# Kernel optimization log

Measured on AMD Instinct MI355X. Metric: run time of the kernel, lower is better.

## Reference

```python
import jax, jax.numpy as jnp
import numpy as np

D_MODEL = 1024
NUM_HEAD = 16
D_HEAD = D_MODEL // NUM_HEAD
D_FFN = 4096
EPS = 1e-6


def setup_inputs() -> dict:
    key = jax.random.key(0)
    ks = jax.random.split(key, 8)
    s = 0.02
    return {
        "x": jax.random.normal(ks[0], (2, 2048, D_MODEL), dtype=jnp.float32),
        "wq": jax.random.normal(ks[1], (D_MODEL, D_MODEL), dtype=jnp.float32) * s,
        "bq": jnp.zeros((D_MODEL,), jnp.float32),
        "ln1_a": jax.random.uniform(ks[2], (D_MODEL,), dtype=jnp.float32),
        "ln1_b": jnp.zeros((D_MODEL,), jnp.float32),
        "ln2_a": jax.random.uniform(ks[3], (D_MODEL,), dtype=jnp.float32),
        "ln2_b": jnp.zeros((D_MODEL,), jnp.float32),
        "w1": jax.random.normal(ks[4], (D_FFN, D_MODEL), dtype=jnp.float32) * s,
        "b1": jnp.zeros((D_FFN,), jnp.float32),
        "w2": jax.random.normal(ks[5], (D_MODEL, D_FFN), dtype=jnp.float32) * s,
        "b2": jnp.zeros((D_MODEL,), jnp.float32),
    }


def _laynorm(x, a, b):
    # torch.std is unbiased (ddof=1); original divides by (std + eps)
    mean = jnp.mean(x, axis=-1, keepdims=True)
    std = jnp.std(x, axis=-1, keepdims=True, ddof=1)
    return a * ((x - mean) / (std + EPS)) + b


def reference(x, wq, bq, ln1_a, ln1_b, ln2_a, ln2_b, w1, b1, w2, b2):
    B, S, D = x.shape
    # NOTE: original applies Wq to Q, K, and V (Wk/Wv unused); Wo never applied.
    h = x @ wq.T + bq                      # [B,S,D]
    h = h.reshape(B, S, NUM_HEAD, D_HEAD)  # q = k = v = h
    scale = 1.0 / jnp.sqrt(jnp.float32(D_HEAD))
    scores = jnp.einsum("bqhd,bkhd->bhqk", h, h) * scale  # [B,H,S,S]
    att = jax.nn.softmax(scores, axis=-1)
    att_out = jnp.einsum("bhqk,bkhd->bqhd", att, h).reshape(B, S, D)
    # dropout is identity at inference
    x1 = _laynorm(x + att_out, ln1_a, ln1_b)
    ffn = jax.nn.relu(x1 @ w1.T + b1) @ w2.T + b2
    return _laynorm(x1 + ffn, ln2_a, ln2_b)
```

## Files before the change

kernel.cpp:

```cpp
#include <hip/hip_runtime.h>

typedef __bf16 bf16v8 __attribute__((ext_vector_type(8)));
typedef float f32x4 __attribute__((ext_vector_type(4)));

#define AS1 __attribute__((address_space(1)))
#define AS3 __attribute__((address_space(3)))

__device__ __forceinline__ void gl_lds16(const void* g, void* s) {
  __builtin_amdgcn_global_load_lds((const AS1 void*)g, (AS3 void*)s, 16, 0, 0);
}

__device__ __forceinline__ unsigned short f2b(float f) {
  union { float f; unsigned u; } v; v.f = f;
  unsigned r = v.u + 0x7fffu + ((v.u >> 16) & 1u);
  return (unsigned short)(r >> 16);
}

__device__ __forceinline__ float bitsf(unsigned u) {
  union { unsigned u; float f; } v; v.u = u;
  return v.f;
}

__global__ __launch_bounds__(256) void cvt_all(const float* __restrict__ x,
                                               const float* __restrict__ wq,
                                               const float* __restrict__ w1,
                                               const float* __restrict__ w2,
                                               unsigned short* __restrict__ xb,
                                               unsigned short* __restrict__ wqb,
                                               unsigned short* __restrict__ w1b,
                                               unsigned short* __restrict__ w2b) {
  int bid = blockIdx.x;
  const float* in;
  unsigned short* out;
  int base;
  if (bid < 4096)       { in = x;  out = xb;  base = bid; }
  else if (bid < 5120)  { in = wq; out = wqb; base = bid - 4096; }
  else if (bid < 9216)  { in = w1; out = w1b; base = bid - 5120; }
  else                  { in = w2; out = w2b; base = bid - 9216; }
  long i = ((long)base * 256 + threadIdx.x) * 4;
  float4 v = *(const float4*)(in + i);
  ushort4 u = make_ushort4(f2b(v.x), f2b(v.y), f2b(v.z), f2b(v.w));
  *(ushort4*)(out + i) = u;
}

template <int RELU, int SPLIT>
__global__ __launch_bounds__(512, 2) void gemm256p(const unsigned short* __restrict__ A,
                                                   const unsigned short* __restrict__ B,
                                                   const float* __restrict__ bias,
                                                   unsigned short* __restrict__ Cb,
                                                   int M, int N, int K, int Ks) {
  __shared__ unsigned short As[2][2][8192];
  __shared__ unsigned short Bs[2][2][8192];

  const int tid = threadIdx.x;
  const int wave = tid >> 6, lane = tid & 63;
  const int wr = wave >> 2, wc = wave & 3;
  const int g = lane >> 4, l15 = lane & 15;

  const int gx = gridDim.x;
  const int nwg = gx * gridDim.y;
  const int lin = blockIdx.y * gx + blockIdx.x;
  const int cpx = nwg >> 3;
  const int swz = (lin & 7) * cpx + (lin >> 3);
  const long m0 = (long)(swz / gx) * 256;
  const long n0 = (long)(swz % gx) * 256;
  const int kBase = blockIdx.z * Ks;

  const int srow = lane >> 2;
  const int schunk = ((lane & 3) ^ ((lane >> 3) & 3)) * 8;

  auto stA = [&](int buf, int kk, int kb) {
#pragma unroll
    for (int j = 0; j < 2; ++j) {
      const int seg = wave * 2 + j;
      gl_lds16(A + (m0 + seg * 16 + srow) * (long)K + kb + kk * 32 + schunk,
               &As[buf][kk][seg * 512]);
    }
  };
  auto stB = [&](int buf, int kk, int kb) {
#pragma unroll
    for (int j = 0; j < 2; ++j) {
      const int seg = wave * 2 + j;
      gl_lds16(B + (n0 + seg * 16 + srow) * (long)K + kb + kk * 32 + schunk,
               &Bs[buf][kk][seg * 512]);
    }
  };

  const int sel = (l15 >> 1) & 3;
  const int colA = (g ^ sel) << 3;

  f32x4 acc[8][4] = {};
  const int nt = Ks >> 6;

  stA(0, 0, kBase); stB(0, 0, kBase); stA(0, 1, kBase); stB(0, 1, kBase);
  asm volatile("s_waitcnt vmcnt(4)" ::: "memory");
  __builtin_amdgcn_s_barrier();

  int cur = 0;
  for (int t = 0; t < nt; ++t) {
    const bool pf = (t + 1 < nt);
    const int kbn = kBase + ((t + 1) << 6);
    bf16v8 af[8], b0, b1, b2, b3;

#pragma unroll
    for (int m = 0; m < 8; ++m)
      af[m] = *(const bf16v8*)&As[cur][0][(wr * 128 + m * 16 + l15) * 32 + colA];
    b0 = *(const bf16v8*)&Bs[cur][0][(wc * 64 + 0 * 16 + l15) * 32 + colA];
    b1 = *(const bf16v8*)&Bs[cur][0][(wc * 64 + 1 * 16 + l15) * 32 + colA];
    if (pf) stA(cur ^ 1, 0, kbn);
    __builtin_amdgcn_s_barrier();
    asm volatile("s_waitcnt lgkmcnt(0)" ::: "memory");
    __builtin_amdgcn_s_setprio(1);
#pragma unroll
    for (int m = 0; m < 8; ++m) {
      acc[m][0] = __builtin_amdgcn_mfma_f32_16x16x32_bf16(af[m], b0, acc[m][0], 0, 0, 0);
      acc[m][1] = __builtin_amdgcn_mfma_f32_16x16x32_bf16(af[m], b1, acc[m][1], 0, 0, 0);
    }
    __builtin_amdgcn_s_setprio(0);
    __builtin_amdgcn_s_barrier();

    b2 = *(const bf16v8*)&Bs[cur][0][(wc * 64 + 2 * 16 + l15) * 32 + colA];
    b3 = *(const bf16v8*)&Bs[cur][0][(wc * 64 + 3 * 16 + l15) * 32 + colA];
    if (pf) stB(cur ^ 1, 0, kbn);
    __builtin_amdgcn_s_barrier();
    asm volatile("s_waitcnt lgkmcnt(0)" ::: "memory");
    __builtin_amdgcn_s_setprio(1);
#pragma unroll
    for (int m = 0; m < 8; ++m) {
      acc[m][2] = __builtin_amdgcn_mfma_f32_16x16x32_bf16(af[m], b2, acc[m][2], 0, 0, 0);
      acc[m][3] = __builtin_amdgcn_mfma_f32_16x16x32_bf16(af[m], b3, acc[m][3], 0, 0, 0);
    }
    __builtin_amdgcn_s_setprio(0);
    if (pf) { asm volatile("s_waitcnt vmcnt(4)" ::: "memory"); }
    else    { asm volatile("s_waitcnt vmcnt(0)" ::: "memory"); }
    __builtin_amdgcn_s_barrier();

#pragma unroll
    for (int m = 0; m < 8; ++m)
      af[m] = *(const bf16v8*)&As[cur][1][(wr * 128 + m * 16 + l15) * 32 + colA];
    b0 = *(const bf16v8*)&Bs[cur][1][(wc * 64 + 0 * 16 + l15) * 32 + colA];
    b1 = *(const bf16v8*)&Bs[cur][1][(wc * 64 + 1 * 16 + l15) * 32 + colA];
    if (pf) stA(cur ^ 1, 1, kbn);
    __builtin_amdgcn_s_barrier();
    asm volatile("s_waitcnt lgkmcnt(0)" ::: "memory");
    __builtin_amdgcn_s_setprio(1);
#pragma unroll
    for (int m = 0; m < 8; ++m) {
      acc[m][0] = __builtin_amdgcn_mfma_f32_16x16x32_bf16(af[m], b0, acc[m][0], 0, 0, 0);
      acc[m][1] = __builtin_amdgcn_mfma_f32_16x16x32_bf16(af[m], b1, acc[m][1], 0, 0, 0);
    }
    __builtin_amdgcn_s_setprio(0);
    __builtin_amdgcn_s_barrier();

    b2 = *(const bf16v8*)&Bs[cur][1][(wc * 64 + 2 * 16 + l15) * 32 + colA];
    b3 = *(const bf16v8*)&Bs[cur][1][(wc * 64 + 3 * 16 + l15) * 32 + colA];
    if (pf) stB(cur ^ 1, 1, kbn);
    __builtin_amdgcn_s_barrier();
    asm volatile("s_waitcnt lgkmcnt(0)" ::: "memory");
    __builtin_amdgcn_s_setprio(1);
#pragma unroll
    for (int m = 0; m < 8; ++m) {
      acc[m][2] = __builtin_amdgcn_mfma_f32_16x16x32_bf16(af[m], b2, acc[m][2], 0, 0, 0);
      acc[m][3] = __builtin_amdgcn_mfma_f32_16x16x32_bf16(af[m], b3, acc[m][3], 0, 0, 0);
    }
    __builtin_amdgcn_s_setprio(0);
    if (pf) { asm volatile("s_waitcnt vmcnt(4)" ::: "memory"); }
    else    { asm volatile("s_waitcnt vmcnt(0)" ::: "memory"); }
    __builtin_amdgcn_s_barrier();

    cur ^= 1;
  }

  const long zoff = SPLIT ? (long)blockIdx.z * M * (long)N : 0;
#pragma unroll
  for (int m = 0; m < 8; ++m)
#pragma unroll
    for (int n = 0; n < 4; ++n) {
      long col = n0 + wc * 64 + n * 16 + l15;
      float bv = SPLIT ? 0.f : bias[col];
      long rowb = m0 + wr * 128 + m * 16 + g * 4;
#pragma unroll
      for (int i = 0; i < 4; ++i) {
        float v = acc[m][n][i] + bv;
        if (RELU) v = fmaxf(v, 0.f);
        Cb[zoff + (rowb + i) * (long)N + col] = f2b(v);
      }
    }
}

__global__ __launch_bounds__(256) void merge4_bias(const unsigned short* __restrict__ p,
                                                   const float* __restrict__ bias,
                                                   unsigned short* __restrict__ out) {
  const long PS = 4096L * 1024L;
  long i = ((long)blockIdx.x * 256 + threadIdx.x) * 8;
  int col = (int)(i & 1023);
  float4 b0 = *(const float4*)(bias + col);
  float4 b1 = *(const float4*)(bias + col + 4);
  float acc[8] = {b0.x, b0.y, b0.z, b0.w, b1.x, b1.y, b1.z, b1.w};
#pragma unroll
  for (int sp = 0; sp < 4; ++sp) {
    uint4 u = *(const uint4*)(p + sp * PS + i);
    unsigned r[4] = {u.x, u.y, u.z, u.w};
#pragma unroll
    for (int j = 0; j < 4; ++j) {
      acc[j * 2]     += bitsf(r[j] << 16);
      acc[j * 2 + 1] += bitsf(r[j] & 0xffff0000u);
    }
  }
  unsigned short res[8];
#pragma unroll
  for (int j = 0; j < 8; ++j) res[j] = f2b(acc[j]);
  *(uint4*)(out + i) = *(uint4*)res;
}

__global__ __launch_bounds__(512, 2) void attn_kernel(const unsigned short* __restrict__ h,
                                                      unsigned short* __restrict__ o) {
  const int id = blockIdx.y * 8 + blockIdx.x;
  const int bh = id & 31;
  const int b = bh >> 4, head = bh & 15;
  const int q0 = (id >> 5) * 256;
  const unsigned short* hb = h + (long)b * 2048 * 1024 + head * 64;

  __shared__ unsigned short smem[2 * 19712];

  const int tid = threadIdx.x, wave = tid >> 6, lane = tid & 63;
  const int grp = wave >> 2, wg = wave & 3;
  const int g = lane >> 4, l15 = lane & 15;
  const int vcb = wg * 16;
  unsigned short* Ks0 = smem + grp * 19712;
  unsigned short* VTb = Ks0 + 8192;

  for (int idx = wg * 64 + lane; idx < 16 * 72; idx += 256) {
    unsigned short v = (idx < 72) ? (unsigned short)0x3F80 : (unsigned short)0;
    VTb[64 * 72 + idx] = v;
    VTb[5760 + 64 * 72 + idx] = v;
  }

  const float C1 = 0.18033688011112042f;

  bf16v8 qf[4][2];
#pragma unroll
  for (int qt = 0; qt < 4; ++qt)
#pragma unroll
    for (int d = 0; d < 2; ++d) {
      bf16v8 q = *(const bf16v8*)(hb + (long)(q0 + wg * 64 + qt * 16 + l15) * 1024 + d * 32 + g * 8);
#pragma unroll
      for (int j = 0; j < 8; ++j) q[j] = (__bf16)((float)q[j] * C1);
      qf[qt][d] = q;
    }

  const int krow = lane >> 3;
  const int kcol = ((lane & 7) ^ (krow & 7)) << 3;

  const int kl = lane;
  const int vpos = ((kl >> 5) << 5) + (((kl & 15) >> 2) << 3) + (((kl >> 4) & 1) << 2) + (kl & 3);

#pragma unroll
  for (int s = 0; s < 2; ++s) {
    int seg = wg * 2 + s;
    gl_lds16(hb + (long)(grp * 64 + seg * 8 + krow) * 1024 + kcol, Ks0 + seg * 512);
  }
  uint4 va0, va1;
  {
    const unsigned short* vg = hb + (long)(grp * 64 + lane) * 1024 + vcb;
    va0 = *(const uint4*)vg;
    va1 = *(const uint4*)(vg + 8);
  }
  {
    unsigned short vv[16];
    *(uint4*)&vv[0] = va0;
    *(uint4*)&vv[8] = va1;
#pragma unroll
    for (int j = 0; j < 16; ++j) VTb[(vcb + j) * 72 + vpos] = vv[j];
  }
  __syncthreads();

  f32x4 accO[4][4] = {};
  f32x4 accL[4] = {};

  int cur = 0;
  for (int t = 0; t < 16; ++t) {
    if (t < 15) {
      const int k0n = ((t + 1) * 2 + grp) * 64;
#pragma unroll
      for (int s = 0; s < 2; ++s) {
        int seg = wg * 2 + s;
        gl_lds16(hb + (long)(k0n + seg * 8 + krow) * 1024 + kcol, Ks0 + (cur ^ 1) * 4096 + seg * 512);
      }
      const unsigned short* vg = hb + (long)(k0n + lane) * 1024 + vcb;
      va0 = *(const uint4*)vg;
      va1 = *(const uint4*)(vg + 8);
    }

    const unsigned short* Kc = Ks0 + cur * 4096;
    f32x4 sf[4][4] = {};
#pragma unroll
    for (int d = 0; d < 2; ++d) {
#pragma unroll
      for (int kt = 0; kt < 4; ++kt) {
        int r = kt * 16 + l15;
        bf16v8 kf = *(const bf16v8*)&Kc[r * 64 + ((((d << 2) + g) ^ (r & 7)) << 3)];
#pragma unroll
        for (int qt = 0; qt < 4; ++qt)
          sf[kt][qt] = __builtin_amdgcn_mfma_f32_16x16x32_bf16(kf, qf[qt][d], sf[kt][qt], 0, 0, 0);
      }
    }

    bf16v8 pa[4][2];
#pragma unroll
    for (int qt = 0; qt < 4; ++qt) {
      float pe[4][4];
#pragma unroll
      for (int kt = 0; kt < 4; ++kt)
#pragma unroll
        for (int i = 0; i < 4; ++i)
          pe[kt][i] = __builtin_amdgcn_exp2f(sf[kt][qt][i]);
#pragma unroll
      for (int i = 0; i < 4; ++i) {
        pa[qt][0][i]     = (__bf16)pe[0][i];
        pa[qt][0][i + 4] = (__bf16)pe[1][i];
        pa[qt][1][i]     = (__bf16)pe[2][i];
        pa[qt][1][i + 4] = (__bf16)pe[3][i];
      }
    }

    const unsigned short* VTc = VTb + cur * 5760;
#pragma unroll
    for (int ks = 0; ks < 2; ++ks) {
      bf16v8 vl = *(const bf16v8*)&VTc[(64 + l15) * 72 + ks * 32 + g * 8];
#pragma unroll
      for (int dt = 0; dt < 4; ++dt) {
        bf16v8 vf = *(const bf16v8*)&VTc[(dt * 16 + l15) * 72 + ks * 32 + g * 8];
#pragma unroll
        for (int qt = 0; qt < 4; ++qt)
          accO[qt][dt] = __builtin_amdgcn_mfma_f32_16x16x32_bf16(pa[qt][ks], vf, accO[qt][dt], 0, 0, 0);
      }
#pragma unroll
      for (int qt = 0; qt < 4; ++qt)
        accL[qt] = __builtin_amdgcn_mfma_f32_16x16x32_bf16(pa[qt][ks], vl, accL[qt], 0, 0, 0);
    }

    if (t < 15) {
      unsigned short vv[16];
      *(uint4*)&vv[0] = va0;
      *(uint4*)&vv[8] = va1;
      unsigned short* VTn = VTb + (cur ^ 1) * 5760;
#pragma unroll
      for (int j = 0; j < 16; ++j) VTn[(vcb + j) * 72 + vpos] = vv[j];
    }
    __syncthreads();
    cur ^= 1;
  }

  float* redO = (float*)smem;
  float* redL = (float*)smem + 16384;
  if (grp == 1) {
#pragma unroll
    for (int qt = 0; qt < 4; ++qt)
#pragma unroll
      for (int i = 0; i < 4; ++i) {
        int r = wg * 64 + qt * 16 + g * 4 + i;
#pragma unroll
        for (int dt = 0; dt < 4; ++dt)
          redO[r * 64 + dt * 16 + l15] = accO[qt][dt][i];
        if (l15 == 0) redL[r] = accL[qt][i];
      }
  }
  __syncthreads();
  if (grp == 0) {
#pragma unroll
    for (int qt = 0; qt < 4; ++qt)
#pragma unroll
      for (int i = 0; i < 4; ++i) {
        int r = wg * 64 + qt * 16 + g * 4 + i;
#pragma unroll
        for (int dt = 0; dt < 4; ++dt)
          accO[qt][dt][i] += redO[r * 64 + dt * 16 + l15];
        accL[qt][i] += redL[r];
      }
#pragma unroll
    for (int qt = 0; qt < 4; ++qt)
#pragma unroll
      for (int i = 0; i < 4; ++i) {
        float linv = 1.f / __shfl(accL[qt][i], lane & 48);
        long row = (long)b * 2048 + q0 + wg * 64 + qt * 16 + g * 4 + i;
#pragma unroll
        for (int dt = 0; dt < 4; ++dt)
          o[row * 1024 + head * 64 + dt * 16 + l15] = f2b(accO[qt][dt][i] * linv);
      }
  }
}

__global__ __launch_bounds__(256) void ln1_attb(const float* __restrict__ xa,
                                                const unsigned short* __restrict__ ab,
                                                const float* __restrict__ g,
                                                const float* __restrict__ be,
                                                float* __restrict__ of,
                                                unsigned short* __restrict__ ob) {
  const long base = (long)blockIdx.x * 1024;
  const int t = threadIdx.x;
  float4 va = *(const float4*)(xa + base + t * 4);
  uint2 ub = *(const uint2*)(ab + base + t * 4);
  float v0 = va.x + bitsf(ub.x << 16);
  float v1 = va.y + bitsf(ub.x & 0xffff0000u);
  float v2 = va.z + bitsf(ub.y << 16);
  float v3 = va.w + bitsf(ub.y & 0xffff0000u);
  float s = v0 + v1 + v2 + v3;
  float sq = v0 * v0 + v1 * v1 + v2 * v2 + v3 * v3;
#pragma unroll
  for (int m = 1; m < 64; m <<= 1) { s += __shfl_xor(s, m); sq += __shfl_xor(sq, m); }
  __shared__ float red[8];
  const int wave = t >> 6, lane = t & 63;
  if (lane == 0) { red[wave] = s; red[4 + wave] = sq; }
  __syncthreads();
  s = red[0] + red[1] + red[2] + red[3];
  sq = red[4] + red[5] + red[6] + red[7];
  float mean = s * (1.f / 1024.f);
  float var = fmaxf(sq - s * mean, 0.f) * (1.f / 1023.f);
  float inv = 1.f / (sqrtf(var) + 1e-6f);
  float4 gg = *(const float4*)(g + t * 4);
  float4 bb = *(const float4*)(be + t * 4);
  float y0 = gg.x * ((v0 - mean) * inv) + bb.x;
  float y1 = gg.y * ((v1 - mean) * inv) + bb.y;
  float y2 = gg.z * ((v2 - mean) * inv) + bb.z;
  float y3 = gg.w * ((v3 - mean) * inv) + bb.w;
  *(float4*)(of + base + t * 4) = make_float4(y0, y1, y2, y3);
  ushort4 u = make_ushort4(f2b(y0), f2b(y1), f2b(y2), f2b(y3));
  *(ushort4*)(ob + base + t * 4) = u;
}

__global__ __launch_bounds__(256) void ln_add_red4(const float* __restrict__ xa,
                                                   const unsigned short* __restrict__ zp,
                                                   const float* __restrict__ bias,
                                                   const float* __restrict__ g,
                                                   const float* __restrict__ be,
                                                   float* __restrict__ of) {
  const long base = (long)blockIdx.x * 1024;
  const int t = threadIdx.x;
  const long PS = 4096L * 1024L;
  float4 va = *(const float4*)(xa + base + t * 4);
  float4 bz = *(const float4*)(bias + t * 4);
  float v0 = va.x + bz.x, v1 = va.y + bz.y, v2 = va.z + bz.z, v3 = va.w + bz.w;
#pragma unroll
  for (int sp = 0; sp < 4; ++sp) {
    uint2 u = *(const uint2*)(zp + sp * PS + base + t * 4);
    v0 += bitsf(u.x << 16);
    v1 += bitsf(u.x & 0xffff0000u);
    v2 += bitsf(u.y << 16);
    v3 += bitsf(u.y & 0xffff0000u);
  }
  float s = v0 + v1 + v2 + v3;
  float sq = v0 * v0 + v1 * v1 + v2 * v2 + v3 * v3;
#pragma unroll
  for (int m = 1; m < 64; m <<= 1) { s += __shfl_xor(s, m); sq += __shfl_xor(sq, m); }
  __shared__ float red[8];
  const int wave = t >> 6, lane = t & 63;
  if (lane == 0) { red[wave] = s; red[4 + wave] = sq; }
  __syncthreads();
  s = red[0] + red[1] + red[2] + red[3];
  sq = red[4] + red[5] + red[6] + red[7];
  float mean = s * (1.f / 1024.f);
  float var = fmaxf(sq - s * mean, 0.f) * (1.f / 1023.f);
  float inv = 1.f / (sqrtf(var) + 1e-6f);
  float4 gg = *(const float4*)(g + t * 4);
  float4 bb = *(const float4*)(be + t * 4);
  float y0 = gg.x * ((v0 - mean) * inv) + bb.x;
  float y1 = gg.y * ((v1 - mean) * inv) + bb.y;
  float y2 = gg.z * ((v2 - mean) * inv) + bb.z;
  float y3 = gg.w * ((v3 - mean) * inv) + bb.w;
  *(float4*)(of + base + t * 4) = make_float4(y0, y1, y2, y3);
}

extern "C" void kernel_launch(void* const* d_in, const int* in_sizes, int n_in,
                              void* d_out, int out_size, void* d_ws, size_t ws_size,
                              hipStream_t stream) {
  const float* x    = (const float*)d_in[0];
  const float* wq   = (const float*)d_in[1];
  const float* bq   = (const float*)d_in[2];
  const float* ln1a = (const float*)d_in[3];
  const float* ln1b = (const float*)d_in[4];
  const float* ln2a = (const float*)d_in[5];
  const float* ln2b = (const float*)d_in[6];
  const float* w1   = (const float*)d_in[7];
  const float* b1   = (const float*)d_in[8];
  const float* w2   = (const float*)d_in[9];
  const float* b2   = (const float*)d_in[10];
  float* out = (float*)d_out;

  char* ws = (char*)d_ws;
  const size_t MB = 1024 * 1024;
  unsigned short* xb  = (unsigned short*)(ws);
  unsigned short* wqb = (unsigned short*)(ws + 8 * MB);
  unsigned short* w1b = (unsigned short*)(ws + 10 * MB);
  unsigned short* w2b = (unsigned short*)(ws + 18 * MB);
  unsigned short* qp  = (unsigned short*)(ws + 26 * MB);
  unsigned short* yb  = (unsigned short*)(ws + 26 * MB);
  unsigned short* hb  = (unsigned short*)(ws + 58 * MB);
  unsigned short* att = (unsigned short*)(ws + 66 * MB);
  unsigned short* zp  = (unsigned short*)(ws + 58 * MB);
  float*          x1f = (float*)(ws + 90 * MB);
  unsigned short* x1b = (unsigned short*)(ws + 106 * MB);

  cvt_all<<<13312, 256, 0, stream>>>(x, wq, w1, w2, xb, wqb, w1b, w2b);

  gemm256p<0, 1><<<dim3(4, 16, 4), 512, 0, stream>>>(xb, wqb, nullptr, qp,
                                                     4096, 1024, 1024, 256);
  merge4_bias<<<2048, 256, 0, stream>>>(qp, bq, hb);

  attn_kernel<<<dim3(8, 32), 512, 0, stream>>>(hb, att);

  ln1_attb<<<4096, 256, 0, stream>>>(x, att, ln1a, ln1b, x1f, x1b);

  gemm256p<1, 0><<<dim3(16, 16, 1), 512, 0, stream>>>(x1b, w1b, b1, yb,
                                                      4096, 4096, 1024, 1024);

  gemm256p<0, 1><<<dim3(4, 16, 4), 512, 0, stream>>>(yb, w2b, nullptr, zp,
                                                     4096, 1024, 4096, 1024);

  ln_add_red4<<<4096, 256, 0, stream>>>(x1f, zp, b2, ln2a, ln2b, out);
}
```

Before: 177.0 us.

## Replace 256x256 GEMM with simpler 256x128 tile, K=32 step double-buffered kernel

Replaces the hand-pipelined 256x256 GEMM, which interleaved MFMA with staged loads under fine-grained barriers, with a simpler 256x128 tile kernel. The new kernel stages A and B at K=32 per step with one barrier per iteration and issues a 4x4 MFMA block per wave. The grids double so there are more workgroups to fill the CUs. In exchange, per-tile data reuse drops and barriers per K become more frequent, and the careful overlap of LDS reads with MFMA is lost.

New measurement: 180.4 us. About the same (+2.0%).

```diff
diff --git a/kernel.cpp b/kernel.cpp
--- a/kernel.cpp
+++ b/kernel.cpp
@@ -44,17 +44,17 @@
 }
 
 template <int RELU, int SPLIT>
-__global__ __launch_bounds__(512, 2) void gemm256p(const unsigned short* __restrict__ A,
-                                                   const unsigned short* __restrict__ B,
-                                                   const float* __restrict__ bias,
-                                                   unsigned short* __restrict__ Cb,
-                                                   int M, int N, int K, int Ks) {
-  __shared__ unsigned short As[2][2][8192];
-  __shared__ unsigned short Bs[2][2][8192];
+__global__ __launch_bounds__(512, 2) void gemm_bn(const unsigned short* __restrict__ A,
+                                                  const unsigned short* __restrict__ B,
+                                                  const float* __restrict__ bias,
+                                                  unsigned short* __restrict__ Cb,
+                                                  int M, int N, int K, int Ks) {
+  __shared__ unsigned short As[2][256 * 32];
+  __shared__ unsigned short Bs[2][128 * 32];
 
   const int tid = threadIdx.x;
   const int wave = tid >> 6, lane = tid & 63;
-  const int wr = wave >> 2, wc = wave & 3;
+  const int wr = wave >> 1, wc = wave & 1;
   const int g = lane >> 4, l15 = lane & 15;
 
   const int gx = gridDim.x;
@@ -63,122 +63,65 @@
   const int cpx = nwg >> 3;
   const int swz = (lin & 7) * cpx + (lin >> 3);
   const long m0 = (long)(swz / gx) * 256;
-  const long n0 = (long)(swz % gx) * 256;
+  const long n0 = (long)(swz % gx) * 128;
   const int kBase = blockIdx.z * Ks;
 
-  const int srow = lane >> 2;
-  const int schunk = ((lane & 3) ^ ((lane >> 3) & 3)) * 8;
-
-  auto stA = [&](int buf, int kk, int kb) {
+  auto stage = [&](int buf, int kb) {
 #pragma unroll
     for (int j = 0; j < 2; ++j) {
-      const int seg = wave * 2 + j;
-      gl_lds16(A + (m0 + seg * 16 + srow) * (long)K + kb + kk * 32 + schunk,
-               &As[buf][kk][seg * 512]);
+      int idx = (j * 8 + wave) * 64 + lane;
+      int row = idx >> 2, p = idx & 3;
+      gl_lds16(A + (m0 + row) * (long)K + kb + ((p ^ ((row >> 1) & 3)) << 3),
+               &As[buf][(j * 8 + wave) * 512]);
+    }
+    {
+      int idx = wave * 64 + lane;
+      int row = idx >> 2, p = idx & 3;
+      gl_lds16(B + (n0 + row) * (long)K + kb + ((p ^ ((row >> 1) & 3)) << 3),
+               &Bs[buf][wave * 512]);
     }
   };
-  auto stB = [&](int buf, int kk, int kb) {
-#pragma unroll
-    for (int j = 0; j < 2; ++j) {
-      const int seg = wave * 2 + j;
-      gl_lds16(B + (n0 + seg * 16 + srow) * (long)K + kb + kk * 32 + schunk,
-               &Bs[buf][kk][seg * 512]);
-    }
-  };
-
-  const int sel = (l15 >> 1) & 3;
-  const int colA = (g ^ sel) << 3;
-
-  f32x4 acc[8][4] = {};
-  const int nt = Ks >> 6;
-
-  stA(0, 0, kBase); stB(0, 0, kBase); stA(0, 1, kBase); stB(0, 1, kBase);
-  asm volatile("s_waitcnt vmcnt(4)" ::: "memory");
-  __builtin_amdgcn_s_barrier();
+
+  f32x4 acc[4][4] = {};
+  const int nt = Ks >> 5;
+
+  stage(0, kBase);
+  __syncthreads();
 
   int cur = 0;
   for (int t = 0; t < nt; ++t) {
-    const bool pf = (t + 1 < nt);
-    const int kbn = kBase + ((t + 1) << 6);
-    bf16v8 af[8], b0, b1, b2, b3;
-
-#pragma unroll
-    for (int m = 0; m < 8; ++m)
-      af[m] = *(const bf16v8*)&As[cur][0][(wr * 128 + m * 16 + l15) * 32 + colA];
-    b0 = *(const bf16v8*)&Bs[cur][0][(wc * 64 + 0 * 16 + l15) * 32 + colA];
-    b1 = *(const bf16v8*)&Bs[cur][0][(wc * 64 + 1 * 16 + l15) * 32 + colA];
-    if (pf) stA(cur ^ 1, 0, kbn);
-    __builtin_amdgcn_s_barrier();
-    asm volatile("s_waitcnt lgkmcnt(0)" ::: "memory");
+    if (t + 1 < nt) stage(cur ^ 1, kBase + ((t + 1) << 5));
+
+    bf16v8 af[4], bn[4];
+#pragma unroll
+    for (int m = 0; m < 4; ++m) {
+      int row = wr * 64 + m * 16 + l15;
+      af[m] = *(const bf16v8*)&As[cur][row * 32 + ((g ^ ((row >> 1) & 3)) << 3)];
+    }
+#pragma unroll
+    for (int n = 0; n < 4; ++n) {
+      int row = wc * 64 + n * 16 + l15;
+      bn[n] = *(const bf16v8*)&Bs[cur][row * 32 + ((g ^ ((row >> 1) & 3)) << 3)];
+    }
     __builtin_amdgcn_s_setprio(1);
 #pragma unroll
-    for (int m = 0; m < 8; ++m) {
-      acc[m][0] = __builtin_amdgcn_mfma_f32_16x16x32_bf16(af[m], b0, acc[m][0], 0, 0, 0);
-      acc[m][1] = __builtin_amdgcn_mfma_f32_16x16x32_bf16(af[m], b1, acc[m][1], 0, 0, 0);
-    }
+    for (int m = 0; m < 4; ++m)
+#pragma unroll
+      for (int n = 0; n < 4; ++n)
+        acc[m][n] = __builtin_amdgcn_mfma_f32_16x16x32_bf16(af[m], bn[n], acc[m][n], 0, 0, 0);
     __builtin_amdgcn_s_setprio(0);
-    __builtin_amdgcn_s_barrier();
-
-    b2 = *(const bf16v8*)&Bs[cur][0][(wc * 64 + 2 * 16 + l15) * 32 + colA];
-    b3 = *(const bf16v8*)&Bs[cur][0][(wc * 64 + 3 * 16 + l15) * 32 + colA];
-    if (pf) stB(cur ^ 1, 0, kbn);
-    __builtin_amdgcn_s_barrier();
-    asm volatile("s_waitcnt lgkmcnt(0)" ::: "memory");
-    __builtin_amdgcn_s_setprio(1);
-#pragma unroll
-    for (int m = 0; m < 8; ++m) {
-      acc[m][2] = __builtin_amdgcn_mfma_f32_16x16x32_bf16(af[m], b2, acc[m][2], 0, 0, 0);
-      acc[m][3] = __builtin_amdgcn_mfma_f32_16x16x32_bf16(af[m], b3, acc[m][3], 0, 0, 0);
-    }
-    __builtin_amdgcn_s_setprio(0);
-    if (pf) { asm volatile("s_waitcnt vmcnt(4)" ::: "memory"); }
-    else    { asm volatile("s_waitcnt vmcnt(0)" ::: "memory"); }
-    __builtin_amdgcn_s_barrier();
-
-#pragma unroll
-    for (int m = 0; m < 8; ++m)
-      af[m] = *(const bf16v8*)&As[cur][1][(wr * 128 + m * 16 + l15) * 32 + colA];
-    b0 = *(const bf16v8*)&Bs[cur][1][(wc * 64 + 0 * 16 + l15) * 32 + colA];
-    b1 = *(const bf16v8*)&Bs[cur][1][(wc * 64 + 1 * 16 + l15) * 32 + colA];
-    if (pf) stA(cur ^ 1, 1, kbn);
-    __builtin_amdgcn_s_barrier();
-    asm volatile("s_waitcnt lgkmcnt(0)" ::: "memory");
-    __builtin_amdgcn_s_setprio(1);
-#pragma unroll
-    for (int m = 0; m < 8; ++m) {
-      acc[m][0] = __builtin_amdgcn_mfma_f32_16x16x32_bf16(af[m], b0, acc[m][0], 0, 0, 0);
-      acc[m][1] = __builtin_amdgcn_mfma_f32_16x16x32_bf16(af[m], b1, acc[m][1], 0, 0, 0);
-    }
-    __builtin_amdgcn_s_setprio(0);
-    __builtin_amdgcn_s_barrier();
-
-    b2 = *(const bf16v8*)&Bs[cur][1][(wc * 64 + 2 * 16 + l15) * 32 + colA];
-    b3 = *(const bf16v8*)&Bs[cur][1][(wc * 64 + 3 * 16 + l15) * 32 + colA];
-    if (pf) stB(cur ^ 1, 1, kbn);
-    __builtin_amdgcn_s_barrier();
-    asm volatile("s_waitcnt lgkmcnt(0)" ::: "memory");
-    __builtin_amdgcn_s_setprio(1);
-#pragma unroll
-    for (int m = 0; m < 8; ++m) {
-      acc[m][2] = __builtin_amdgcn_mfma_f32_16x16x32_bf16(af[m], b2, acc[m][2], 0, 0, 0);
-      acc[m][3] = __builtin_amdgcn_mfma_f32_16x16x32_bf16(af[m], b3, acc[m][3], 0, 0, 0);
-    }
-    __builtin_amdgcn_s_setprio(0);
-    if (pf) { asm volatile("s_waitcnt vmcnt(4)" ::: "memory"); }
-    else    { asm volatile("s_waitcnt vmcnt(0)" ::: "memory"); }
-    __builtin_amdgcn_s_barrier();
-
+    __syncthreads();
     cur ^= 1;
   }
 
   const long zoff = SPLIT ? (long)blockIdx.z * M * (long)N : 0;
 #pragma unroll
-  for (int m = 0; m < 8; ++m)
+  for (int m = 0; m < 4; ++m)
 #pragma unroll
     for (int n = 0; n < 4; ++n) {
       long col = n0 + wc * 64 + n * 16 + l15;
       float bv = SPLIT ? 0.f : bias[col];
-      long rowb = m0 + wr * 128 + m * 16 + g * 4;
+      long rowb = m0 + wr * 64 + m * 16 + g * 4;
 #pragma unroll
       for (int i = 0; i < 4; ++i) {
         float v = acc[m][n][i] + bv;
@@ -503,19 +446,19 @@
 
   cvt_all<<<13312, 256, 0, stream>>>(x, wq, w1, w2, xb, wqb, w1b, w2b);
 
-  gemm256p<0, 1><<<dim3(4, 16, 4), 512, 0, stream>>>(xb, wqb, nullptr, qp,
-                                                     4096, 1024, 1024, 256);
+  gemm_bn<0, 1><<<dim3(8, 16, 4), 512, 0, stream>>>(xb, wqb, nullptr, qp,
+                                                    4096, 1024, 1024, 256);
   merge4_bias<<<2048, 256, 0, stream>>>(qp, bq, hb);
 
   attn_kernel<<<dim3(8, 32), 512, 0, stream>>>(hb, att);
 
   ln1_attb<<<4096, 256, 0, stream>>>(x, att, ln1a, ln1b, x1f, x1b);
 
-  gemm256p<1, 0><<<dim3(16, 16, 1), 512, 0, stream>>>(x1b, w1b, b1, yb,
-                                                      4096, 4096, 1024, 1024);
-
-  gemm256p<0, 1><<<dim3(4, 16, 4), 512, 0, stream>>>(yb, w2b, nullptr, zp,
-                                                     4096, 1024, 4096, 1024);
+  gemm_bn<1, 0><<<dim3(32, 16, 1), 512, 0, stream>>>(x1b, w1b, b1, yb,
+                                                     4096, 4096, 1024, 1024);
+
+  gemm_bn<0, 1><<<dim3(8, 16, 4), 512, 0, stream>>>(yb, w2b, nullptr, zp,
+                                                    4096, 1024, 4096, 1024);
 
   ln_add_red4<<<4096, 256, 0, stream>>>(x1f, zp, b2, ln2a, ln2b, out);
 }
```
